# Kernel optimization log

Hardware: AMD Instinct MI355X
Metric: run time of the kernel (lower is better)

The kernel has to match this reference:

```python
import jax, jax.numpy as jnp
import numpy as np
from jax import lax

HID, STATE, K, EXPAND = 1024, 16, 4, 2
INNER = EXPAND * HID
B_SZ, L = 4, 4096


def setup_inputs() -> dict:
    key = jax.random.key(0)
    ks = jax.random.split(key, 16)
    s = 0.02
    return {
        "x": jax.random.normal(ks[0], (B_SZ, L, HID), dtype=jnp.float32),
        "in_proj_w": jax.random.normal(ks[1], (2 * INNER, HID), dtype=jnp.float32) * s,
        "in_proj_b": jnp.zeros((2 * INNER,), jnp.float32),
        "conv_w": jax.random.normal(ks[2], (INNER, 1, K), dtype=jnp.float32) * s,
        "conv_b": jnp.zeros((INNER,), jnp.float32),
        "dt_w": jax.random.normal(ks[3], (INNER, INNER), dtype=jnp.float32) * s,
        "dt_b": jnp.zeros((INNER,), jnp.float32),
        "A_log": jnp.log(jnp.abs(jax.random.normal(ks[4], (INNER, STATE), dtype=jnp.float32)) + 1e-6),
        "B_w": jax.random.normal(ks[5], (STATE, INNER), dtype=jnp.float32) * s,
        "B_b": jnp.zeros((STATE,), jnp.float32),
        "C_w": jax.random.normal(ks[6], (STATE, INNER), dtype=jnp.float32) * s,
        "C_b": jnp.zeros((STATE,), jnp.float32),
        "D": jnp.ones((INNER,), jnp.float32),
        "out_w": jax.random.normal(ks[7], (HID, INNER), dtype=jnp.float32) * s,
        "out_b": jnp.zeros((HID,), jnp.float32),
    }


def _selective_scan(x, dt, A, Bm, Cm, D):
    # x, dt: (B, L, inner); A: (inner, state); Bm, Cm: (B, L, state); D: (inner,)
    def step(h, inp):
        x_t, dt_t, B_t, C_t = inp  # (B,inner),(B,inner),(B,state),(B,state)
        dA = jnp.exp(dt_t[:, :, None] * A[None, :, :])          # (B, inner, state)
        dB = dt_t[:, :, None] * B_t[:, None, :]                  # (B, inner, state)
        h = dA * h + dB * x_t[:, :, None]
        y = jnp.einsum("bds,bs->bd", h, C_t) + D * x_t
        return h, y

    B_, _, d = x.shape
    h0 = jnp.zeros((B_, d, A.shape[1]), x.dtype)
    xs = (jnp.swapaxes(x, 0, 1), jnp.swapaxes(dt, 0, 1),
          jnp.swapaxes(Bm, 0, 1), jnp.swapaxes(Cm, 0, 1))
    _, ys = lax.scan(step, h0, xs)  # ys: (L, B, inner)
    return jnp.swapaxes(ys, 0, 1)


def reference(x, in_proj_w, in_proj_b, conv_w, conv_b, dt_w, dt_b,
              A_log, B_w, B_b, C_w, C_b, D, out_w, out_b):
    xz = x @ in_proj_w.T + in_proj_b                 # (B, L, 2*inner)
    x_part, z = jnp.split(xz, 2, axis=-1)
    # causal depthwise conv1d: torch pads both sides K-1 then truncates to L -> left pad only
    xc = lax.conv_general_dilated(
        jnp.swapaxes(x_part, 1, 2), conv_w,
        window_strides=(1,), padding=[(K - 1, 0)],
        dimension_numbers=("NCH", "OIH", "NCH"),
        feature_group_count=INNER) + conv_b[None, :, None]
    x_conv = jax.nn.silu(jnp.swapaxes(xc, 1, 2))     # (B, L, inner)
    A = -jnp.exp(A_log)
    dt = jax.nn.softplus(x_conv @ dt_w.T + dt_b)
    Bm = x_conv @ B_w.T + B_b                        # (B, L, state)
    Cm = x_conv @ C_w.T + C_b
    y = _selective_scan(x_conv, dt, A, Bm, Cm, D)
    y = y * jax.nn.silu(z)
    return y @ out_w.T + out_b
```

## Files before the change

### kernel.cpp

```cpp
#include <hip/hip_runtime.h>
#include <hip/hip_bf16.h>

#define HID   1024
#define STATE 16
#define KCONV 4
#define INNER 2048
#define BSZ   4
#define LSEQ  4096
#define BL    (BSZ * LSEQ)
#define NCAT  2304
#define NCH   64
#define TC    64

typedef unsigned short ushort_t;
typedef unsigned int   uint_t;
typedef __attribute__((ext_vector_type(8))) __bf16 bf16x8;
typedef __attribute__((ext_vector_type(4))) float  f32x4;
typedef __attribute__((ext_vector_type(8))) unsigned short u16x8;

__device__ __forceinline__ ushort_t f2bf(float f) {
    uint_t u = __float_as_uint(f);
    u += 0x7fffu + ((u >> 16) & 1u);
    return (ushort_t)(u >> 16);
}
__device__ __forceinline__ float bf2f(ushort_t h) {
    return __uint_as_float(((uint_t)h) << 16);
}

#define AS1 __attribute__((address_space(1)))
#define AS3 __attribute__((address_space(3)))
__device__ __forceinline__ void async_copy16(const ushort_t* g, ushort_t* l) {
    __builtin_amdgcn_global_load_lds((const AS1 void*)g, (AS3 void*)l, 16, 0, 0);
}

__global__ void cast_bf16_kernel(const float* __restrict__ src, ushort_t* __restrict__ dst, int n) {
    int i = blockIdx.x * 256 + threadIdx.x;
    if (i < n) dst[i] = f2bf(src[i]);
}

__global__ void build_wcat_kernel(const float* __restrict__ dtw, const float* __restrict__ Bw,
                                  const float* __restrict__ Cw, ushort_t* __restrict__ out) {
    int i = blockIdx.x * 256 + threadIdx.x;
    if (i >= NCAT * INNER) return;
    int r = i >> 11;
    int k = i & (INNER - 1);
    float v = 0.f;
    if (r < INNER)            v = dtw[i];
    else if (r < INNER + 16)  v = Bw[(r - INNER) * INNER + k];
    else if (r < INNER + 32)  v = Cw[(r - INNER - 16) * INNER + k];
    out[i] = f2bf(v);
}

__global__ void build_biascat_kernel(const float* __restrict__ dtb, const float* __restrict__ Bb,
                                     const float* __restrict__ Cb, float* __restrict__ out) {
    int i = blockIdx.x * 256 + threadIdx.x;
    if (i >= NCAT) return;
    float v = 0.f;
    if (i < INNER)            v = dtb[i];
    else if (i < INNER + 16)  v = Bb[i - INNER];
    else if (i < INNER + 32)  v = Cb[i - INNER - 16];
    out[i] = v;
}

#define mfma_bf16 __builtin_amdgcn_mfma_f32_16x16x32_bf16

template <int MODE>
__global__ __launch_bounds__(512, 2) void gemm256_kernel(
    const ushort_t* __restrict__ A, const ushort_t* __restrict__ Bw,
    const float* __restrict__ bias,
    ushort_t* __restrict__ oU0, ushort_t* __restrict__ oU1,
    float* __restrict__ oF, float* __restrict__ oB, float* __restrict__ oC,
    int N, int K)
{
    __shared__ ushort_t smem[65536];

    const int tid  = threadIdx.x;
    const int w    = tid >> 6;
    const int lane = tid & 63;
    const int m16  = lane & 15;
    const int ko   = lane >> 4;
    const int wm   = w >> 2;
    const int wn   = w & 3;
    const int wnh  = wn >> 1;

    const int gx   = gridDim.x;
    const int lb   = blockIdx.y * gx + blockIdx.x;
    const int xcd  = lb & 7;
    const int slot = lb >> 3;
    const int tx   = slot % gx;
    const int ty   = xcd * 8 + slot / gx;
    const int row0 = ty * 256;
    const int col0 = tx * 256;

    const int nkt  = K >> 6;
    const int HMAX = nkt << 2;

    const ushort_t* gA = A  + (size_t)row0 * K;
    const ushort_t* gB = Bw + (size_t)col0 * K;

    f32x4 acc[8][4] = {};

    auto stage_half = [&](int h) {
        const int tau = h >> 2, j = h & 3;
        const int sbase = ((tau & 1) << 15) | (j << 13);
        const ushort_t* src = (j < 2) ? gB + (size_t)(j << 7) * K
                                      : gA + (size_t)((j - 2) << 7) * K;
        const int k0 = tau << 6;
#pragma unroll
        for (int i = 0; i < 2; i++) {
            const int boff = w * 2048 + i * 1024 + lane * 16;
            const int row  = boff >> 7;
            const int c16  = (boff >> 4) & 7;
            const ushort_t* s = src + (size_t)row * K + k0 + ((c16 ^ (row & 7)) << 3);
            async_copy16(s, &smem[sbase + w * 1024 + i * 512]);
        }
    };
    auto ldA = [&](int buf, int rf, int s) -> bf16x8 {
        const int row = (rf << 4) + m16;
        const int c16 = ((s << 2) + ko) ^ (row & 7);
        return *(const bf16x8*)&smem[(buf << 15) + ((2 + wm) << 13) + (row << 6) + (c16 << 3)];
    };
    auto ldB = [&](int buf, int cf, int s) -> bf16x8 {
        const int row = ((wn & 1) << 6) + (cf << 4) + m16;
        const int c16 = ((s << 2) + ko) ^ (row & 7);
        return *(const bf16x8*)&smem[(buf << 15) + (wnh << 13) + (row << 6) + (c16 << 3)];
    };

    for (int h = 0; h < 6; ++h) stage_half(h);
    asm volatile("s_waitcnt vmcnt(4)" ::: "memory");
    __builtin_amdgcn_s_barrier();

    int h = 6;
    for (int t = 0; t < nkt; ++t) {
        const int buf = t & 1;
        bf16x8 aF[4][2], bC0[2][2], bC1[2][2];

#pragma unroll
        for (int r = 0; r < 4; r++) { aF[r][0] = ldA(buf, r, 0); aF[r][1] = ldA(buf, r, 1); }
#pragma unroll
        for (int c = 0; c < 2; c++) { bC0[c][0] = ldB(buf, c, 0); bC0[c][1] = ldB(buf, c, 1); }
        if (h < HMAX) stage_half(h);
        ++h;
        __builtin_amdgcn_s_barrier();
        __builtin_amdgcn_s_setprio(1);
#pragma unroll
        for (int r = 0; r < 4; r++)
#pragma unroll
            for (int c = 0; c < 2; c++) {
                acc[r][c] = mfma_bf16(aF[r][0], bC0[c][0], acc[r][c], 0, 0, 0);
                acc[r][c] = mfma_bf16(aF[r][1], bC0[c][1], acc[r][c], 0, 0, 0);
            }
        __builtin_amdgcn_s_setprio(0);
        __builtin_amdgcn_s_barrier();

#pragma unroll
        for (int c = 0; c < 2; c++) { bC1[c][0] = ldB(buf, 2 + c, 0); bC1[c][1] = ldB(buf, 2 + c, 1); }
        if (h < HMAX) stage_half(h);
        ++h;
        __builtin_amdgcn_s_barrier();
        __builtin_amdgcn_s_setprio(1);
#pragma unroll
        for (int r = 0; r < 4; r++)
#pragma unroll
            for (int c = 0; c < 2; c++) {
                acc[r][2 + c] = mfma_bf16(aF[r][0], bC1[c][0], acc[r][2 + c], 0, 0, 0);
                acc[r][2 + c] = mfma_bf16(aF[r][1], bC1[c][1], acc[r][2 + c], 0, 0, 0);
            }
        __builtin_amdgcn_s_setprio(0);
        __builtin_amdgcn_s_barrier();

#pragma unroll
        for (int r = 0; r < 4; r++) { aF[r][0] = ldA(buf, 4 + r, 0); aF[r][1] = ldA(buf, 4 + r, 1); }
        if (h < HMAX) stage_half(h);
        ++h;
        __builtin_amdgcn_s_barrier();
        __builtin_amdgcn_s_setprio(1);
#pragma unroll
        for (int r = 0; r < 4; r++)
#pragma unroll
            for (int c = 0; c < 2; c++) {
                acc[4 + r][2 + c] = mfma_bf16(aF[r][0], bC1[c][0], acc[4 + r][2 + c], 0, 0, 0);
                acc[4 + r][2 + c] = mfma_bf16(aF[r][1], bC1[c][1], acc[4 + r][2 + c], 0, 0, 0);
            }
        __builtin_amdgcn_s_setprio(0);
        __builtin_amdgcn_s_barrier();

        if (h < HMAX) stage_half(h);
        ++h;
        __builtin_amdgcn_s_barrier();
        __builtin_amdgcn_s_setprio(1);
#pragma unroll
        for (int r = 0; r < 4; r++)
#pragma unroll
            for (int c = 0; c < 2; c++) {
                acc[4 + r][c] = mfma_bf16(aF[r][0], bC0[c][0], acc[4 + r][c], 0, 0, 0);
                acc[4 + r][c] = mfma_bf16(aF[r][1], bC0[c][1], acc[4 + r][c], 0, 0, 0);
            }
        __builtin_amdgcn_s_setprio(0);
        if (t + 1 < nkt) {
            if (t + 1 == nkt - 1) asm volatile("s_waitcnt vmcnt(0)" ::: "memory");
            else                  asm volatile("s_waitcnt vmcnt(4)" ::: "memory");
            __builtin_amdgcn_s_barrier();
        }
    }

    const int rbase = (lane >> 4) * 4;
#pragma unroll
    for (int i = 0; i < 8; i++) {
#pragma unroll
        for (int j = 0; j < 4; j++) {
#pragma unroll
            for (int r = 0; r < 4; r++) {
                int row = row0 + wm * 128 + i * 16 + rbase + r;
                int col = col0 + wn * 64 + j * 16 + m16;
                float v = acc[i][j][r] + bias[col];
                if (MODE == 0) {
                    if (col < INNER) {
                        oU0[(size_t)row * INNER + col] = f2bf(v);
                    } else {
                        float s = v / (1.f + __expf(-v));
                        oU1[(size_t)row * INNER + (col - INNER)] = f2bf(s);
                    }
                } else if (MODE == 1) {
                    if (col < INNER) {
                        float sp = fmaxf(v, 0.f) + log1pf(__expf(-fabsf(v)));
                        oU0[(size_t)row * INNER + col] = f2bf(sp);
                    } else if (col < INNER + 16) {
                        oB[(size_t)row * STATE + (col - INNER)] = v;
                    } else if (col < INNER + 32) {
                        oC[(size_t)row * STATE + (col - INNER - 16)] = v;
                    }
                } else {
                    oF[(size_t)row * N + col] = v;
                }
            }
        }
    }
}

__global__ void conv_silu_kernel(const ushort_t* __restrict__ xp, const float* __restrict__ cw,
                                 const float* __restrict__ cb,
                                 ushort_t* __restrict__ xcbf) {
    int i = blockIdx.x * 256 + threadIdx.x;
    int base = i * 8;
    int d0 = base & (INNER - 1);
    int bl = base >> 11;
    int l  = bl & (LSEQ - 1);

    f32x4 wv[8];
    float acc[8];
#pragma unroll
    for (int j = 0; j < 8; j++) {
        wv[j]  = *(const f32x4*)&cw[(d0 + j) * KCONV];
        acc[j] = cb[d0 + j];
    }
#pragma unroll
    for (int k = 0; k < KCONV; k++) {
        int ls = l - (KCONV - 1) + k;
        if (ls >= 0) {
            u16x8 v = *(const u16x8*)&xp[base + (ls - l) * INNER];
#pragma unroll
            for (int j = 0; j < 8; j++) acc[j] = fmaf(wv[j][k], bf2f(v[j]), acc[j]);
        }
    }
    u16x8 o;
#pragma unroll
    for (int j = 0; j < 8; j++) {
        float s = acc[j] / (1.f + __expf(-acc[j]));
        o[j] = f2bf(s);
    }
    *(u16x8*)&xcbf[base] = o;
}

__global__ __launch_bounds__(256) void scan_pass1(
    const ushort_t* __restrict__ dt, const ushort_t* __restrict__ xc,
    const float* __restrict__ Bm, const float* __restrict__ A_log,
    ushort_t* __restrict__ Pc, float* __restrict__ Sc)
{
    const int b = blockIdx.z;
    const int c = blockIdx.y;
    const int d = blockIdx.x * 256 + threadIdx.x;

    float A[STATE], h[STATE];
    {
        float al[STATE];
#pragma unroll
        for (int q = 0; q < 4; q++)
            *(f32x4*)(al + q * 4) = *(const f32x4*)(A_log + (size_t)d * STATE + q * 4);
#pragma unroll
        for (int s = 0; s < STATE; s++) { A[s] = -__expf(al[s]); h[s] = 0.f; }
    }
    float sdt = 0.f;
    const size_t base = (size_t)b * LSEQ + (size_t)c * TC;

#pragma unroll 2
    for (int t = 0; t < TC; t++) {
        const size_t r = base + t;
        const float dtv = bf2f(dt[r * INNER + d]);
        const float xv  = bf2f(xc[r * INNER + d]);
        const float dtx = dtv * xv;
        float Bv[STATE];
#pragma unroll
        for (int q = 0; q < 4; q++)
            *(f32x4*)(Bv + q * 4) = *(const f32x4*)(Bm + r * STATE + q * 4);
        sdt += dtv;
#pragma unroll
        for (int s = 0; s < STATE; s++) {
            const float dA = __expf(dtv * A[s]);
            h[s] = fmaf(dA, h[s], dtx * Bv[s]);
        }
    }

    const size_t idx = ((size_t)(b * NCH + c) * INNER + d) * STATE;
#pragma unroll
    for (int q = 0; q < 4; q++)
        *(f32x4*)(Sc + idx + q * 4) = *(const f32x4*)(h + q * 4);
    u16x8 p0, p1;
#pragma unroll
    for (int s = 0; s < 8; s++) { p0[s] = f2bf(__expf(A[s] * sdt)); }
#pragma unroll
    for (int s = 0; s < 8; s++) { p1[s] = f2bf(__expf(A[s + 8] * sdt)); }
    *(u16x8*)(Pc + idx)     = p0;
    *(u16x8*)(Pc + idx + 8) = p1;
}

__global__ __launch_bounds__(256) void scan_pass2(
    const ushort_t* __restrict__ Pc, float* Sc)
{
    const int i = blockIdx.x * 256 + threadIdx.x;
    const int b   = i >> 15;
    const int rem = i & (INNER * STATE - 1);
    float H = 0.f;
#pragma unroll 8
    for (int c = 0; c < NCH; c++) {
        const size_t idx = (size_t)(b * NCH + c) * (INNER * STATE) + rem;
        const float Pv = bf2f(Pc[idx]);
        const float Sv = Sc[idx];
        const float Hn = fmaf(Pv, H, Sv);
        Sc[idx] = H;
        H = Hn;
    }
}

__global__ __launch_bounds__(256) void scan_pass3(
    const ushort_t* __restrict__ dt, const ushort_t* __restrict__ xc,
    const float* __restrict__ Bm, const float* __restrict__ Cm,
    const float* __restrict__ A_log, const float* __restrict__ Dv,
    const float* __restrict__ Hc, ushort_t* sz_y)
{
    const int b = blockIdx.z;
    const int c = blockIdx.y;
    const int d = blockIdx.x * 256 + threadIdx.x;

    float A[STATE], h[STATE];
    {
        float al[STATE];
#pragma unroll
        for (int q = 0; q < 4; q++)
            *(f32x4*)(al + q * 4) = *(const f32x4*)(A_log + (size_t)d * STATE + q * 4);
#pragma unroll
        for (int s = 0; s < STATE; s++) A[s] = -__expf(al[s]);
    }
    const size_t hidx = ((size_t)(b * NCH + c) * INNER + d) * STATE;
#pragma unroll
    for (int q = 0; q < 4; q++)
        *(f32x4*)(h + q * 4) = *(const f32x4*)(Hc + hidx + q * 4);

    const float Dd = Dv[d];
    const size_t base = (size_t)b * LSEQ + (size_t)c * TC;

#pragma unroll 2
    for (int t = 0; t < TC; t++) {
        const size_t r = base + t;
        const float dtv = bf2f(dt[r * INNER + d]);
        const float xv  = bf2f(xc[r * INNER + d]);
        const float dtx = dtv * xv;
        float Bv[STATE], Cv[STATE];
#pragma unroll
        for (int q = 0; q < 4; q++) {
            *(f32x4*)(Bv + q * 4) = *(const f32x4*)(Bm + r * STATE + q * 4);
            *(f32x4*)(Cv + q * 4) = *(const f32x4*)(Cm + r * STATE + q * 4);
        }
        float y = Dd * xv;
#pragma unroll
        for (int s = 0; s < STATE; s++) {
            const float dA = __expf(dtv * A[s]);
            h[s] = fmaf(dA, h[s], dtx * Bv[s]);
            y = fmaf(h[s], Cv[s], y);
        }
        const float zv = bf2f(sz_y[r * INNER + d]);
        sz_y[r * INNER + d] = f2bf(y * zv);
    }
}

extern "C" void kernel_launch(void* const* d_in, const int* in_sizes, int n_in,
                              void* d_out, int out_size, void* d_ws, size_t ws_size,
                              hipStream_t stream) {
    const float* x       = (const float*)d_in[0];
    const float* in_w    = (const float*)d_in[1];
    const float* in_b    = (const float*)d_in[2];
    const float* conv_w  = (const float*)d_in[3];
    const float* conv_b  = (const float*)d_in[4];
    const float* dt_w    = (const float*)d_in[5];
    const float* dt_b    = (const float*)d_in[6];
    const float* A_log   = (const float*)d_in[7];
    const float* B_w     = (const float*)d_in[8];
    const float* B_b     = (const float*)d_in[9];
    const float* C_w     = (const float*)d_in[10];
    const float* C_b     = (const float*)d_in[11];
    const float* Dv      = (const float*)d_in[12];
    const float* out_w   = (const float*)d_in[13];
    const float* out_b   = (const float*)d_in[14];
    float* out = (float*)d_out;

    char* ws = (char*)d_ws;
    size_t off = 0;
    auto alloc = [&](size_t bytes) { size_t o = off; off += (bytes + 255) & ~(size_t)255; return o; };

    ushort_t* Xbf     = (ushort_t*)(ws + alloc((size_t)BL * HID * 2));
    ushort_t* W1bf    = (ushort_t*)(ws + alloc((size_t)2 * INNER * HID * 2));
    ushort_t* Wcat    = (ushort_t*)(ws + alloc((size_t)NCAT * INNER * 2));
    ushort_t* Woutbf  = (ushort_t*)(ws + alloc((size_t)HID * INNER * 2));
    float*    biascat = (float*)   (ws + alloc((size_t)NCAT * 4));
    ushort_t* xpart   = (ushort_t*)(ws + alloc((size_t)BL * INNER * 2));
    ushort_t* szbf    = (ushort_t*)(ws + alloc((size_t)BL * INNER * 2));
    ushort_t* xconvbf = (ushort_t*)(ws + alloc((size_t)BL * INNER * 2));
    float*    Bmbuf   = (float*)   (ws + alloc((size_t)BL * STATE * 4));
    float*    Cmbuf   = (float*)   (ws + alloc((size_t)BL * STATE * 4));
    ushort_t* dtbuf   = xpart;

    ushort_t* Pbuf = (ushort_t*)ws;
    float*    Sbuf = (float*)(ws + (size_t)NCH * BSZ * INNER * STATE * 2);
    (void)in_sizes; (void)n_in; (void)out_size;

    if (ws_size < off) return;

    {
        int n = BL * HID;
        cast_bf16_kernel<<<(n + 255) / 256, 256, 0, stream>>>(x, Xbf, n);
        n = 2 * INNER * HID;
        cast_bf16_kernel<<<(n + 255) / 256, 256, 0, stream>>>(in_w, W1bf, n);
        n = HID * INNER;
        cast_bf16_kernel<<<(n + 255) / 256, 256, 0, stream>>>(out_w, Woutbf, n);
        n = NCAT * INNER;
        build_wcat_kernel<<<(n + 255) / 256, 256, 0, stream>>>(dt_w, B_w, C_w, Wcat);
        build_biascat_kernel<<<(NCAT + 255) / 256, 256, 0, stream>>>(dt_b, B_b, C_b, biascat);
    }

    gemm256_kernel<0><<<dim3((2 * INNER) / 256, BL / 256), 512, 0, stream>>>(
        Xbf, W1bf, in_b, xpart, szbf, nullptr, nullptr, nullptr, 2 * INNER, HID);

    conv_silu_kernel<<<(BL * INNER / 8) / 256, 256, 0, stream>>>(xpart, conv_w, conv_b, xconvbf);

    gemm256_kernel<1><<<dim3(NCAT / 256, BL / 256), 512, 0, stream>>>(
        xconvbf, Wcat, biascat, dtbuf, nullptr, nullptr, Bmbuf, Cmbuf, NCAT, INNER);

    scan_pass1<<<dim3(INNER / 256, NCH, BSZ), 256, 0, stream>>>(
        dtbuf, xconvbf, Bmbuf, A_log, Pbuf, Sbuf);
    scan_pass2<<<(BSZ * INNER * STATE) / 256, 256, 0, stream>>>(Pbuf, Sbuf);
    scan_pass3<<<dim3(INNER / 256, NCH, BSZ), 256, 0, stream>>>(
        dtbuf, xconvbf, Bmbuf, Cmbuf, A_log, Dv, Sbuf, szbf);

    gemm256_kernel<2><<<dim3(HID / 256, BL / 256), 512, 0, stream>>>(
        szbf, Woutbf, out_b, nullptr, nullptr, out, nullptr, nullptr, HID, INNER);
}
```

Before: 1.090 ms.

## Template GEMM on K, precompute load offsets, stage bf16 epilogue through LDS

The GEMM now takes K as a template parameter and precomputes per-lane global load offsets, which simplifies address arithmetic in the staging loop. The bf16 output epilogues for modes 0 and 1 first write results into shared memory, then issue 16-byte vectorized row stores in place of scattered 2-byte stores. Mode 1 blocks that only hold the B/C columns take a separate path. This adds an extra barrier and an LDS round trip in exchange for coalesced global writes.

```diff
diff --git a/kernel.cpp b/kernel.cpp
--- a/kernel.cpp
+++ b/kernel.cpp
@@ -64,13 +64,13 @@
 
 #define mfma_bf16 __builtin_amdgcn_mfma_f32_16x16x32_bf16
 
-template <int MODE>
+template <int MODE, int KK>
 __global__ __launch_bounds__(512, 2) void gemm256_kernel(
     const ushort_t* __restrict__ A, const ushort_t* __restrict__ Bw,
     const float* __restrict__ bias,
     ushort_t* __restrict__ oU0, ushort_t* __restrict__ oU1,
     float* __restrict__ oF, float* __restrict__ oB, float* __restrict__ oC,
-    int N, int K)
+    int N)
 {
     __shared__ ushort_t smem[65536];
 
@@ -92,27 +92,22 @@
     const int row0 = ty * 256;
     const int col0 = tx * 256;
 
-    const int nkt  = K >> 6;
-    const int HMAX = nkt << 2;
-
-    const ushort_t* gA = A  + (size_t)row0 * K;
-    const ushort_t* gB = Bw + (size_t)col0 * K;
+    constexpr int NKT = KK >> 6;
+
+    const size_t Lofs = (size_t)(w * 16 + (lane >> 3)) * KK
+                      + (size_t)(((lane & 7) ^ (lane >> 3)) << 3);
+    const ushort_t* pA = A  + (size_t)row0 * KK + Lofs;
+    const ushort_t* pB = Bw + (size_t)col0 * KK + Lofs;
 
     f32x4 acc[8][4] = {};
 
-    auto stage_half = [&](int h) {
-        const int tau = h >> 2, j = h & 3;
-        const int sbase = ((tau & 1) << 15) | (j << 13);
-        const ushort_t* src = (j < 2) ? gB + (size_t)(j << 7) * K
-                                      : gA + (size_t)((j - 2) << 7) * K;
-        const int k0 = tau << 6;
+    auto stage_half = [&](int j, int tau) {
+        const int sb = ((tau & 1) << 15) | (j << 13);
+        const ushort_t* px = (j < 2) ? pB : pA;
 #pragma unroll
         for (int i = 0; i < 2; i++) {
-            const int boff = w * 2048 + i * 1024 + lane * 16;
-            const int row  = boff >> 7;
-            const int c16  = (boff >> 4) & 7;
-            const ushort_t* s = src + (size_t)row * K + k0 + ((c16 ^ (row & 7)) << 3);
-            async_copy16(s, &smem[sbase + w * 1024 + i * 512]);
+            const ushort_t* s = px + (size_t)((j & 1) * 128 + i * 8) * KK + (tau << 6);
+            async_copy16(s, &smem[sb + w * 1024 + i * 512]);
         }
     };
     auto ldA = [&](int buf, int rf, int s) -> bf16x8 {
@@ -126,12 +121,13 @@
         return *(const bf16x8*)&smem[(buf << 15) + (wnh << 13) + (row << 6) + (c16 << 3)];
     };
 
-    for (int h = 0; h < 6; ++h) stage_half(h);
+    stage_half(0, 0); stage_half(1, 0); stage_half(2, 0); stage_half(3, 0);
+    stage_half(0, 1); stage_half(1, 1);
     asm volatile("s_waitcnt vmcnt(4)" ::: "memory");
     __builtin_amdgcn_s_barrier();
 
-    int h = 6;
-    for (int t = 0; t < nkt; ++t) {
+#pragma unroll 1
+    for (int t = 0; t < NKT; ++t) {
         const int buf = t & 1;
         bf16x8 aF[4][2], bC0[2][2], bC1[2][2];
 
@@ -139,8 +135,7 @@
         for (int r = 0; r < 4; r++) { aF[r][0] = ldA(buf, r, 0); aF[r][1] = ldA(buf, r, 1); }
 #pragma unroll
         for (int c = 0; c < 2; c++) { bC0[c][0] = ldB(buf, c, 0); bC0[c][1] = ldB(buf, c, 1); }
-        if (h < HMAX) stage_half(h);
-        ++h;
+        if (t + 1 < NKT) stage_half(2, t + 1);
         __builtin_amdgcn_s_barrier();
         __builtin_amdgcn_s_setprio(1);
 #pragma unroll
@@ -155,8 +150,7 @@
 
 #pragma unroll
         for (int c = 0; c < 2; c++) { bC1[c][0] = ldB(buf, 2 + c, 0); bC1[c][1] = ldB(buf, 2 + c, 1); }
-        if (h < HMAX) stage_half(h);
-        ++h;
+        if (t + 1 < NKT) stage_half(3, t + 1);
         __builtin_amdgcn_s_barrier();
         __builtin_amdgcn_s_setprio(1);
 #pragma unroll
@@ -171,8 +165,7 @@
 
 #pragma unroll
         for (int r = 0; r < 4; r++) { aF[r][0] = ldA(buf, 4 + r, 0); aF[r][1] = ldA(buf, 4 + r, 1); }
-        if (h < HMAX) stage_half(h);
-        ++h;
+        if (t + 2 < NKT) stage_half(0, t + 2);
         __builtin_amdgcn_s_barrier();
         __builtin_amdgcn_s_setprio(1);
 #pragma unroll
@@ -185,8 +178,7 @@
         __builtin_amdgcn_s_setprio(0);
         __builtin_amdgcn_s_barrier();
 
-        if (h < HMAX) stage_half(h);
-        ++h;
+        if (t + 2 < NKT) stage_half(1, t + 2);
         __builtin_amdgcn_s_barrier();
         __builtin_amdgcn_s_setprio(1);
 #pragma unroll
@@ -197,43 +189,78 @@
                 acc[4 + r][c] = mfma_bf16(aF[r][1], bC0[c][1], acc[4 + r][c], 0, 0, 0);
             }
         __builtin_amdgcn_s_setprio(0);
-        if (t + 1 < nkt) {
-            if (t + 1 == nkt - 1) asm volatile("s_waitcnt vmcnt(0)" ::: "memory");
+        if (t + 1 < NKT) {
+            if (t + 1 == NKT - 1) asm volatile("s_waitcnt vmcnt(0)" ::: "memory");
             else                  asm volatile("s_waitcnt vmcnt(4)" ::: "memory");
             __builtin_amdgcn_s_barrier();
         }
     }
 
     const int rbase = (lane >> 4) * 4;
-#pragma unroll
-    for (int i = 0; i < 8; i++) {
-#pragma unroll
-        for (int j = 0; j < 4; j++) {
-#pragma unroll
-            for (int r = 0; r < 4; r++) {
-                int row = row0 + wm * 128 + i * 16 + rbase + r;
-                int col = col0 + wn * 64 + j * 16 + m16;
-                float v = acc[i][j][r] + bias[col];
-                if (MODE == 0) {
-                    if (col < INNER) {
-                        oU0[(size_t)row * INNER + col] = f2bf(v);
-                    } else {
-                        float s = v / (1.f + __expf(-v));
-                        oU1[(size_t)row * INNER + (col - INNER)] = f2bf(s);
+    __syncthreads();
+
+    if (MODE == 2) {
+#pragma unroll
+        for (int i = 0; i < 8; i++)
+#pragma unroll
+            for (int j = 0; j < 4; j++)
+#pragma unroll
+                for (int r = 0; r < 4; r++) {
+                    int row = row0 + wm * 128 + i * 16 + rbase + r;
+                    int col = col0 + wn * 64 + j * 16 + m16;
+                    oF[(size_t)row * N + col] = acc[i][j][r] + bias[col];
+                }
+    } else if (MODE == 1 && col0 >= INNER) {
+#pragma unroll
+        for (int i = 0; i < 8; i++)
+#pragma unroll
+            for (int j = 0; j < 4; j++)
+#pragma unroll
+                for (int r = 0; r < 4; r++) {
+                    int row = row0 + wm * 128 + i * 16 + rbase + r;
+                    int col = col0 + wn * 64 + j * 16 + m16;
+                    float v = acc[i][j][r] + bias[col];
+                    if (col < INNER + 16)      oB[(size_t)row * STATE + (col - INNER)] = v;
+                    else if (col < INNER + 32) oC[(size_t)row * STATE + (col - INNER - 16)] = v;
+                }
+    } else {
+        const bool isZ = (MODE == 0) && (col0 >= INNER);
+        ushort_t* my = &smem[w * 8192];
+        const int SW = 68;
+#pragma unroll
+        for (int p = 0; p < 2; p++) {
+#pragma unroll
+            for (int i4 = 0; i4 < 4; i4++)
+#pragma unroll
+                for (int j = 0; j < 4; j++)
+#pragma unroll
+                    for (int r = 0; r < 4; r++) {
+                        int lr = i4 * 16 + rbase + r;
+                        int lc = j * 16 + m16;
+                        float v = acc[p * 4 + i4][j][r] + bias[col0 + wn * 64 + lc];
+                        ushort_t o;
+                        if (MODE == 0) {
+                            if (isZ) { float s = v / (1.f + __expf(-v)); o = f2bf(s); }
+                            else     { o = f2bf(v); }
+                        } else {
+                            float sp = fmaxf(v, 0.f) + log1pf(__expf(-fabsf(v)));
+                            o = f2bf(sp);
+                        }
+                        my[lr * SW + lc] = o;
                     }
-                } else if (MODE == 1) {
-                    if (col < INNER) {
-                        float sp = fmaxf(v, 0.f) + log1pf(__expf(-fabsf(v)));
-                        oU0[(size_t)row * INNER + col] = f2bf(sp);
-                    } else if (col < INNER + 16) {
-                        oB[(size_t)row * STATE + (col - INNER)] = v;
-                    } else if (col < INNER + 32) {
-                        oC[(size_t)row * STATE + (col - INNER - 16)] = v;
-                    }
-                } else {
-                    oF[(size_t)row * N + col] = v;
-                }
+            __builtin_amdgcn_sched_barrier(0);
+#pragma unroll
+            for (int it = 0; it < 8; it++) {
+                int lr = it * 8 + (lane >> 3);
+                u16x8 vv = *(const u16x8*)&my[lr * SW + (lane & 7) * 8];
+                int grow = row0 + wm * 128 + p * 64 + lr;
+                int gcol = col0 + wn * 64 + (lane & 7) * 8;
+                if (MODE == 0 && isZ)
+                    *(u16x8*)&oU1[(size_t)grow * INNER + (gcol - INNER)] = vv;
+                else
+                    *(u16x8*)&oU0[(size_t)grow * INNER + gcol] = vv;
             }
+            __builtin_amdgcn_sched_barrier(0);
         }
     }
 }
@@ -447,13 +474,13 @@
         build_biascat_kernel<<<(NCAT + 255) / 256, 256, 0, stream>>>(dt_b, B_b, C_b, biascat);
     }
 
-    gemm256_kernel<0><<<dim3((2 * INNER) / 256, BL / 256), 512, 0, stream>>>(
-        Xbf, W1bf, in_b, xpart, szbf, nullptr, nullptr, nullptr, 2 * INNER, HID);
+    gemm256_kernel<0, HID><<<dim3((2 * INNER) / 256, BL / 256), 512, 0, stream>>>(
+        Xbf, W1bf, in_b, xpart, szbf, nullptr, nullptr, nullptr, 2 * INNER);
 
     conv_silu_kernel<<<(BL * INNER / 8) / 256, 256, 0, stream>>>(xpart, conv_w, conv_b, xconvbf);
 
-    gemm256_kernel<1><<<dim3(NCAT / 256, BL / 256), 512, 0, stream>>>(
-        xconvbf, Wcat, biascat, dtbuf, nullptr, nullptr, Bmbuf, Cmbuf, NCAT, INNER);
+    gemm256_kernel<1, INNER><<<dim3(NCAT / 256, BL / 256), 512, 0, stream>>>(
+        xconvbf, Wcat, biascat, dtbuf, nullptr, nullptr, Bmbuf, Cmbuf, NCAT);
 
     scan_pass1<<<dim3(INNER / 256, NCH, BSZ), 256, 0, stream>>>(
         dtbuf, xconvbf, Bmbuf, A_log, Pbuf, Sbuf);
@@ -461,6 +488,6 @@
     scan_pass3<<<dim3(INNER / 256, NCH, BSZ), 256, 0, stream>>>(
         dtbuf, xconvbf, Bmbuf, Cmbuf, A_log, Dv, Sbuf, szbf);
 
-    gemm256_kernel<2><<<dim3(HID / 256, BL / 256), 512, 0, stream>>>(
-        szbf, Woutbf, out_b, nullptr, nullptr, out, nullptr, nullptr, HID, INNER);
-}
+    gemm256_kernel<2, INNER><<<dim3(HID / 256, BL / 256), 512, 0, stream>>>(
+        szbf, Woutbf, out_b, nullptr, nullptr, out, nullptr, nullptr, HID);
+}
```

New measurement: 1.032 ms. 5.3% less time.
